# Optimization experiments

Measured on AMD Instinct MI355X. Metric: run time of the kernel, lower is better.

The kernel has to match this reference:

```python
import jax, jax.numpy as jnp
import numpy as np

B, VD, SD, CD, H, HEADS = 16384, 2048, 1024, 512, 256, 4
DH = H // HEADS
EPS = 1e-5


def layer_norm(x, g, b):
    m = jnp.mean(x, axis=-1, keepdims=True)
    v = jnp.var(x, axis=-1, keepdims=True)
    return (x - m) * jax.lax.rsqrt(v + EPS) * g + b


def setup_inputs() -> dict:
    key = jax.random.key(0)
    ks = jax.random.split(key, 16)
    sc = 0.02
    inp = {
        'fv': jax.random.normal(ks[0], (B, VD), jnp.float32),
        'fs': jax.random.normal(ks[1], (B, SD), jnp.float32),
        'fc': jax.random.normal(ks[2], (B, CD), jnp.float32),
        # projection linears + layernorms
        'Wv': jax.random.normal(ks[3], (H, VD), jnp.float32) * sc,
        'bv': jnp.zeros((H,), jnp.float32),
        'gv': jnp.ones((H,), jnp.float32), 'bev': jnp.zeros((H,), jnp.float32),
        'Ws': jax.random.normal(ks[4], (H, SD), jnp.float32) * sc,
        'bs': jnp.zeros((H,), jnp.float32),
        'gs': jnp.ones((H,), jnp.float32), 'bes': jnp.zeros((H,), jnp.float32),
        'Wc': jax.random.normal(ks[5], (H, CD), jnp.float32) * sc,
        'bc': jnp.zeros((H,), jnp.float32),
        'gc_': jnp.ones((H,), jnp.float32), 'bec': jnp.zeros((H,), jnp.float32),
        # MultiheadAttention packed in-proj and out-proj
        'in_w': jax.random.normal(ks[6], (3 * H, H), jnp.float32) * sc,
        'in_b': jnp.zeros((3 * H,), jnp.float32),
        'out_w': jax.random.normal(ks[7], (H, H), jnp.float32) * sc,
        'out_b': jnp.zeros((H,), jnp.float32),
        # post-attention layernorm
        'gn': jnp.ones((H,), jnp.float32), 'gb': jnp.zeros((H,), jnp.float32),
        # gating MLP: Linear(3H,64) -> GELU -> Linear(64,3) -> softmax
        'g1w': jax.random.normal(ks[8], (64, 3 * H), jnp.float32) * sc,
        'g1b': jnp.zeros((64,), jnp.float32),
        'g2w': jax.random.normal(ks[9], (3, 64), jnp.float32) * sc,
        'g2b': jnp.zeros((3,), jnp.float32),
    }
    return inp


def reference(fv, fs, fc, Wv, bv, gv, bev, Ws, bs, gs, bes, Wc, bc, gc_, bec,
              in_w, in_b, out_w, out_b, gn, gb, g1w, g1b, g2w, g2b):
    v = layer_norm(fv @ Wv.T + bv, gv, bev)   # [B,H]
    s = layer_norm(fs @ Ws.T + bs, gs, bes)
    c = layer_norm(fc @ Wc.T + bc, gc_, bec)
    stack = jnp.stack([v, s, c], axis=1)      # [B,3,H]

    # self-attention over seq=3 (eval mode: dropout off)
    qkv = stack @ in_w.T + in_b               # [B,3,3H]
    q, k, vv = jnp.split(qkv, 3, axis=-1)
    def heads(x):  # [B,3,H] -> [B,HEADS,3,DH]
        return x.reshape(B, 3, HEADS, DH).transpose(0, 2, 1, 3)
    q, k, vv = heads(q), heads(k), heads(vv)
    scores = jnp.einsum('bhqd,bhkd->bhqk', q, k) / jnp.sqrt(jnp.float32(DH))
    attn = jax.nn.softmax(scores, axis=-1)
    ctx = jnp.einsum('bhqk,bhkd->bhqd', attn, vv)
    ctx = ctx.transpose(0, 2, 1, 3).reshape(B, 3, H)
    attended = ctx @ out_w.T + out_b          # [B,3,H]

    attended = layer_norm(attended + stack, gn, gb)
    av, as_, ac = attended[:, 0], attended[:, 1], attended[:, 2]

    h1 = jax.nn.gelu(jnp.concatenate([av, as_, ac], axis=-1) @ g1w.T + g1b, approximate=False)
    gates = jax.nn.softmax(h1 @ g2w.T + g2b, axis=-1)  # [B,3]

    fused = gates[:, 0:1] * av + gates[:, 1:2] * as_ + gates[:, 2:3] * ac
    return (fused, gates)
```

## Files before the change

### kernel.cpp

```cpp
#include <hip/hip_runtime.h>
#include <math.h>


typedef unsigned short u16;
typedef __bf16 bf16x8 __attribute__((ext_vector_type(8)));
typedef float fx4 __attribute__((ext_vector_type(4)));

#define MFMA_BF16(A_, B_, C_) __builtin_amdgcn_mfma_f32_16x16x32_bf16((A_), (B_), (C_), 0, 0, 0)
#define WAIT_VM(N) asm volatile("s_waitcnt vmcnt(" #N ")" ::: "memory")

__device__ __forceinline__ float bf2f(u16 s) {
    union { float f; unsigned u; } c; c.u = ((unsigned)s) << 16; return c.f;
}
__device__ __forceinline__ u16 f2bf(float f) {
    union { float f; unsigned u; } c; c.f = f;
    return (u16)((c.u + 0x7fffu + ((c.u >> 16) & 1u)) >> 16);
}
__device__ __forceinline__ float bfpair_dot(unsigned a, unsigned b) {
    union { unsigned u; float f; } al, ah, bl, bh;
    al.u = a << 16; ah.u = a & 0xffff0000u;
    bl.u = b << 16; bh.u = b & 0xffff0000u;
    return al.f * bl.f + ah.f * bh.f;
}
__device__ __forceinline__ void gld16(void* l, const void* g) {
    __builtin_amdgcn_global_load_lds((const __attribute__((address_space(1))) void*)g,
                                     (__attribute__((address_space(3))) void*)l, 16, 0, 0);
}

__global__ __launch_bounds__(256) void cvt_w(const float* Wv, const float* Ws, const float* Wc,
                                             const float* inw, const float* outw, const float* g1w,
                                             u16* dst) {
    int idx = blockIdx.x * 256 + threadIdx.x;
    const float* src; int rel;
    if      (idx <  524288) { src = Wv;   rel = idx; }
    else if (idx <  786432) { src = Ws;   rel = idx -  524288; }
    else if (idx <  917504) { src = Wc;   rel = idx -  786432; }
    else if (idx < 1114112) { src = inw;  rel = idx -  917504; }
    else if (idx < 1179648) { src = outw; rel = idx - 1114112; }
    else                    { src = g1w;  rel = idx - 1179648; }
    dst[idx] = f2bf(src[rel]);
}

__global__ __launch_bounds__(256, 3) void gemm_ln(
    const float* fv, const float* fs, const float* fc,
    const u16* wWv, const u16* wWs, const u16* wWc,
    const float* bv, const float* gv, const float* bev,
    const float* bs, const float* gs, const float* bes,
    const float* bc, const float* gc_, const float* bec,
    u16* stack) {
    __shared__ alignas(16) char smem[45568];
    u16* sC = (u16*)smem;
    float* redS = (float*)(smem + 43008);
    float* redQ = (float*)(smem + 44032);
    float* mvS  = (float*)(smem + 45056);

    int bid = blockIdx.x;
    int slot, mblk;
    if (bid < 256)      { slot = 0; mblk = bid; }
    else if (bid < 512) { slot = 1; mblk = bid - 256; }
    else                { slot = 2; mblk = bid - 512; }

    const float* A; const u16* W; const float* bias; const float* gg; const float* be; int K;
    if (slot == 0)      { A = fv; W = wWv; bias = bv; gg = gv;  be = bev; K = 2048; }
    else if (slot == 1) { A = fs; W = wWs; bias = bs; gg = gs;  be = bes; K = 1024; }
    else                { A = fc; W = wWc; bias = bc; gg = gc_; be = bec; K = 512;  }

    int t = threadIdx.x, wv = t >> 6, ln = t & 63, q = ln >> 4, l15 = ln & 15;
    int m0 = mblk * 64;

    fx4 zero = {0.f, 0.f, 0.f, 0.f};
    fx4 acc[4][4];
    #pragma unroll
    for (int mi = 0; mi < 4; ++mi)
        #pragma unroll
        for (int ni = 0; ni < 4; ++ni) acc[mi][ni] = zero;

    int rowA = t >> 2, ca = t & 3;
    const float* aBase = A + (size_t)(m0 + rowA) * K + ca * 8;
    int sAwOff = rowA * 40 + ca * 8;

    int bN[4], bKc[4], bDst[4];
    #pragma unroll
    for (int i = 0; i < 4; ++i) {
        int d = wv * 256 + i * 64 + ln;
        bN[i] = d >> 2;
        bKc[i] = (d & 3) ^ ((bN[i] >> 1) & 3);
        bDst[i] = (wv * 256 + i * 64) * 16;
    }

    int niter = K >> 5;

    {
        float4 f0 = *(const float4*)(aBase);
        float4 f1 = *(const float4*)(aBase + 4);
        #pragma unroll
        for (int i = 0; i < 4; ++i)
            gld16(smem + 10240 + bDst[i], W + (size_t)bN[i] * K + bKc[i] * 8);
        union { u16 us[8]; uint4 v; } pk;
        pk.us[0] = f2bf(f0.x); pk.us[1] = f2bf(f0.y); pk.us[2] = f2bf(f0.z); pk.us[3] = f2bf(f0.w);
        pk.us[4] = f2bf(f1.x); pk.us[5] = f2bf(f1.y); pk.us[6] = f2bf(f1.z); pk.us[7] = f2bf(f1.w);
        *(uint4*)((u16*)smem + sAwOff) = pk.v;
    }
    __syncthreads();

    for (int kt = 0; kt < niter; ++kt) {
        int cur = kt & 1, nxt_b = (kt + 1) & 1;
        u16* sAc = (u16*)(smem + cur * 5120);
        u16* sBc = (u16*)(smem + 10240 + cur * 16384);
        int has_next = (kt + 1) < niter;

        float4 nf0, nf1;
        if (has_next) {
            nf0 = *(const float4*)(aBase + (kt + 1) * 32);
            nf1 = *(const float4*)(aBase + (kt + 1) * 32 + 4);
            char* sBn = smem + 10240 + nxt_b * 16384;
            #pragma unroll
            for (int i = 0; i < 4; ++i)
                gld16(sBn + bDst[i], W + (size_t)bN[i] * K + (kt + 1) * 32 + bKc[i] * 8);
        }

        bf16x8 af[4], bfr[4];
        #pragma unroll
        for (int mi = 0; mi < 4; ++mi)
            af[mi] = *(const bf16x8*)(sAc + (mi * 16 + l15) * 40 + q * 8);
        #pragma unroll
        for (int ni = 0; ni < 4; ++ni) {
            int n = wv * 64 + ni * 16 + l15;
            int ch = n * 4 + (q ^ ((n >> 1) & 3));
            bfr[ni] = *(const bf16x8*)(sBc + ch * 8);
        }
        #pragma unroll
        for (int mi = 0; mi < 4; ++mi)
            #pragma unroll
            for (int ni = 0; ni < 4; ++ni)
                acc[mi][ni] = MFMA_BF16(af[mi], bfr[ni], acc[mi][ni]);

        if (has_next) {
            union { u16 us[8]; uint4 v; } pk;
            pk.us[0] = f2bf(nf0.x); pk.us[1] = f2bf(nf0.y); pk.us[2] = f2bf(nf0.z); pk.us[3] = f2bf(nf0.w);
            pk.us[4] = f2bf(nf1.x); pk.us[5] = f2bf(nf1.y); pk.us[6] = f2bf(nf1.z); pk.us[7] = f2bf(nf1.w);
            *(uint4*)((u16*)(smem + nxt_b * 5120) + sAwOff) = pk.v;
        }
        __syncthreads();
    }

    float biasv[4], gvv[4], bevv[4];
    #pragma unroll
    for (int ni = 0; ni < 4; ++ni) {
        int col = wv * 64 + ni * 16 + l15;
        biasv[ni] = bias[col]; gvv[ni] = gg[col]; bevv[ni] = be[col];
    }
    #pragma unroll
    for (int mi = 0; mi < 4; ++mi)
        #pragma unroll
        for (int ni = 0; ni < 4; ++ni)
            #pragma unroll
            for (int r = 0; r < 4; ++r) acc[mi][ni][r] += biasv[ni];
    #pragma unroll
    for (int mi = 0; mi < 4; ++mi) {
        #pragma unroll
        for (int r = 0; r < 4; ++r) {
            float s = 0.f, qq = 0.f;
            #pragma unroll
            for (int ni = 0; ni < 4; ++ni) { float x = acc[mi][ni][r]; s += x; qq += x * x; }
            #pragma unroll
            for (int m = 1; m < 16; m <<= 1) { s += __shfl_xor(s, m, 64); qq += __shfl_xor(qq, m, 64); }
            if (l15 == 0) { int rho = mi * 16 + q * 4 + r; redS[rho * 4 + wv] = s; redQ[rho * 4 + wv] = qq; }
        }
    }
    __syncthreads();
    if (t < 64) {
        float s = redS[t * 4] + redS[t * 4 + 1] + redS[t * 4 + 2] + redS[t * 4 + 3];
        float qq = redQ[t * 4] + redQ[t * 4 + 1] + redQ[t * 4 + 2] + redQ[t * 4 + 3];
        float mean = s * (1.f / 256.f);
        float var = qq * (1.f / 256.f) - mean * mean;
        mvS[t * 2] = mean; mvS[t * 2 + 1] = rsqrtf(var + 1e-5f);
    }
    __syncthreads();
    #pragma unroll
    for (int mi = 0; mi < 4; ++mi) {
        #pragma unroll
        for (int r = 0; r < 4; ++r) {
            int rho = mi * 16 + q * 4 + r;
            float mean = mvS[rho * 2], rstd = mvS[rho * 2 + 1];
            #pragma unroll
            for (int ni = 0; ni < 4; ++ni) {
                int col = wv * 64 + ni * 16 + l15;
                float x = (acc[mi][ni][r] - mean) * rstd * gvv[ni] + bevv[ni];
                sC[rho * 256 + col] = f2bf(x);
            }
        }
    }
    __syncthreads();
    u16* outp = stack + (size_t)m0 * 768 + slot * 256;
    #pragma unroll
    for (int it = 0; it < 8; ++it) {
        int idx = t + it * 256;
        int row = idx >> 5, c = idx & 31;
        uint4 v = *(const uint4*)(sC + row * 256 + c * 8);
        *(uint4*)(outp + (size_t)row * 768 + c * 8) = v;
    }
}

__global__ __launch_bounds__(256, 3) void gemm_qkv(const u16* stack, const u16* W, const float* in_b,
                                                   u16* qkv) {
    __shared__ alignas(16) char smem[49152];
    u16* sC = (u16*)smem;

    int t = threadIdx.x, wv = t >> 6, ln = t & 63, q = ln >> 4, l15 = ln & 15;
    int n0 = blockIdx.x * 128, m0 = blockIdx.y * 128;
    int wr = wv >> 1, wc = wv & 1;

    fx4 zero = {0.f, 0.f, 0.f, 0.f};
    fx4 acc[4][4];
    #pragma unroll
    for (int mi = 0; mi < 4; ++mi)
        #pragma unroll
        for (int ni = 0; ni < 4; ++ni) acc[mi][ni] = zero;

    int sR[2], sKc[2];
    #pragma unroll
    for (int i = 0; i < 2; ++i) {
        int d = wv * 128 + i * 64 + ln;
        sR[i] = d >> 2;
        sKc[i] = (d & 3) ^ ((sR[i] >> 1) & 3);
    }

#define QK_ISSUE(ktile, bufoff)                                                         \
    {                                                                                   \
        char* bA_ = smem + (bufoff);                                                    \
        char* bB_ = bA_ + 8192;                                                         \
        _Pragma("unroll")                                                               \
        for (int i_ = 0; i_ < 2; ++i_) {                                                \
            gld16(bA_ + (wv * 128 + i_ * 64) * 16,                                      \
                  stack + (size_t)(m0 + sR[i_]) * 256 + (ktile) * 32 + sKc[i_] * 8);    \
            gld16(bB_ + (wv * 128 + i_ * 64) * 16,                                      \
                  W + (size_t)(n0 + sR[i_]) * 256 + (ktile) * 32 + sKc[i_] * 8);        \
        }                                                                               \
    }

    QK_ISSUE(0, 0);
    QK_ISSUE(1, 16384);
    int cb = 0;
    for (int kt = 0; kt < 8; ++kt) {
        if (kt < 7) { WAIT_VM(4); } else { WAIT_VM(0); }
        __builtin_amdgcn_sched_barrier(0);
        __builtin_amdgcn_s_barrier();
        __builtin_amdgcn_sched_barrier(0);
        int nb = cb + 2; if (nb >= 3) nb -= 3;
        if (kt + 2 < 8) QK_ISSUE(kt + 2, nb * 16384);

        const u16* sAc = (const u16*)(smem + cb * 16384);
        const u16* sBc = (const u16*)(smem + cb * 16384 + 8192);
        bf16x8 af[4], bfr[4];
        #pragma unroll
        for (int mi = 0; mi < 4; ++mi) {
            int r = wr * 64 + mi * 16 + l15;
            int ch = r * 4 + (q ^ ((r >> 1) & 3));
            af[mi] = *(const bf16x8*)(sAc + ch * 8);
        }
        #pragma unroll
        for (int ni = 0; ni < 4; ++ni) {
            int n = wc * 64 + ni * 16 + l15;
            int ch = n * 4 + (q ^ ((n >> 1) & 3));
            bfr[ni] = *(const bf16x8*)(sBc + ch * 8);
        }
        __builtin_amdgcn_s_setprio(1);
        #pragma unroll
        for (int mi = 0; mi < 4; ++mi)
            #pragma unroll
            for (int ni = 0; ni < 4; ++ni)
                acc[mi][ni] = MFMA_BF16(af[mi], bfr[ni], acc[mi][ni]);
        __builtin_amdgcn_s_setprio(0);
        cb += 1; if (cb >= 3) cb -= 3;
    }
#undef QK_ISSUE
    __syncthreads();

    float biasv[4];
    #pragma unroll
    for (int ni = 0; ni < 4; ++ni) biasv[ni] = in_b[n0 + wc * 64 + ni * 16 + l15];
    #pragma unroll
    for (int mi = 0; mi < 4; ++mi)
        #pragma unroll
        for (int ni = 0; ni < 4; ++ni)
            #pragma unroll
            for (int r = 0; r < 4; ++r) {
                int rl = wr * 64 + mi * 16 + q * 4 + r;
                int cl = wc * 64 + ni * 16 + l15;
                sC[rl * 128 + cl] = f2bf(acc[mi][ni][r] + biasv[ni]);
            }
    __syncthreads();
    #pragma unroll
    for (int it = 0; it < 8; ++it) {
        int idx = t + it * 256;
        int row = idx >> 4, c = idx & 15;
        uint4 v = *(const uint4*)(sC + row * 128 + c * 8);
        *(uint4*)(qkv + (size_t)(m0 + row) * 768 + n0 + c * 8) = v;
    }
}

__global__ __launch_bounds__(256) void outproj_k(
    const u16* qkv, const u16* W, const float* out_b, const u16* stack,
    const float* gn, const float* gb, const u16* g1w, const float* g1b,
    const float* g2w, const float* g2b, float* outF, float* outG) {
    __shared__ alignas(16) char smem[65536];
    u16* qk  = (u16*)smem;
    u16* vb  = (u16*)smem;
    u16* r1  = (u16*)(smem + 24576);
    u16* sB  = (u16*)(smem + 49152);
    float* sS   = (float*)(smem + 49152);
    float* redS = (float*)(smem + 49152);
    float* redQ = (float*)(smem + 49920);
    float* mvS  = (float*)(smem + 50688);
    float* h1S  = (float*)(smem + 51072);
    float* lgS  = (float*)(smem + 55168);
    float* gateS= (float*)(smem + 55360);

    int t = threadIdx.x, wv = t >> 6, ln = t & 63, q = ln >> 4, l15 = ln & 15;
    int gr0 = blockIdx.x * 48, b0 = blockIdx.x * 16;

    #pragma unroll
    for (int i = 0; i < 12; ++i) {
        int d = i * 256 + t;
        int row = d >> 6, cc = d & 63;
        gld16((char*)smem + d * 16, qkv + (size_t)(gr0 + row) * 768 + cc * 8);
    }
    __syncthreads();
    #pragma unroll
    for (int it = 0; it < 3; ++it) {
        int idx = t + it * 256;
        if (idx < 576) {
            int b = idx / 36, rem = idx % 36, h = rem / 9, pp = rem % 9, i = pp / 3, j = pp % 3;
            const u16* qp = qk + (b * 3 + i) * 512 + h * 64;
            const u16* kp = qk + (b * 3 + j) * 512 + 256 + h * 64;
            float acc = 0.f;
            #pragma unroll
            for (int c = 0; c < 8; ++c) {
                uint4 qa = *(const uint4*)(qp + c * 8);
                uint4 ka = *(const uint4*)(kp + c * 8);
                acc += bfpair_dot(qa.x, ka.x) + bfpair_dot(qa.y, ka.y) +
                       bfpair_dot(qa.z, ka.z) + bfpair_dot(qa.w, ka.w);
            }
            sS[idx] = acc * 0.125f;
        }
    }
    __syncthreads();
    #pragma unroll
    for (int i = 0; i < 6; ++i) {
        int d = i * 256 + t;
        int row = d >> 5, cc = d & 31;
        gld16((char*)smem + d * 16, qkv + (size_t)(gr0 + row) * 768 + 512 + cc * 8);
    }
    if (t < 192) {
        int b3 = t * 3;
        float s0 = sS[b3], s1 = sS[b3 + 1], s2 = sS[b3 + 2];
        float m = fmaxf(s0, fmaxf(s1, s2));
        float e0 = __expf(s0 - m), e1 = __expf(s1 - m), e2 = __expf(s2 - m);
        float inv = 1.f / (e0 + e1 + e2);
        sS[b3] = e0 * inv; sS[b3 + 1] = e1 * inv; sS[b3 + 2] = e2 * inv;
    }
    __syncthreads();
    #pragma unroll
    for (int it = 0; it < 6; ++it) {
        int idx = t + it * 256;
        int b = idx / 96, rem = idx % 96, i = rem / 32, c = rem & 31, h = c >> 3;
        int pbase = b * 36 + h * 9 + i * 3;
        float o[8];
        #pragma unroll
        for (int e = 0; e < 8; ++e) o[e] = 0.f;
        #pragma unroll
        for (int j = 0; j < 3; ++j) {
            float p = sS[pbase + j];
            uint4 va = *(const uint4*)(vb + (b * 3 + j) * 256 + c * 8);
            unsigned uu[4] = {va.x, va.y, va.z, va.w};
            #pragma unroll
            for (int pr = 0; pr < 4; ++pr) {
                union { unsigned u; float f; } lo, hi;
                lo.u = uu[pr] << 16; hi.u = uu[pr] & 0xffff0000u;
                o[2 * pr]     += p * lo.f;
                o[2 * pr + 1] += p * hi.f;
            }
        }
        union { u16 us[8]; uint4 v; } pk;
        #pragma unroll
        for (int e = 0; e < 8; ++e) pk.us[e] = f2bf(o[e]);
        int row = b * 3 + i;
        *(uint4*)(r1 + (row * 32 + (c ^ (row & 7))) * 8) = pk.v;
    }
    __syncthreads();

    fx4 zero = {0.f, 0.f, 0.f, 0.f};
    fx4 acc[3][4];
    #pragma unroll
    for (int mi = 0; mi < 3; ++mi)
        #pragma unroll
        for (int ni = 0; ni < 4; ++ni) acc[mi][ni] = zero;

    for (int kt = 0; kt < 8; ++kt) {
        #pragma unroll
        for (int i = 0; i < 4; ++i) {
            int d = wv * 256 + i * 64 + ln;
            int n = d >> 2, p = d & 3;
            int kc = p ^ ((n >> 1) & 3);
            gld16((char*)sB + (wv * 256 + i * 64) * 16, W + (size_t)n * 256 + kt * 32 + kc * 8);
        }
        __syncthreads();
        bf16x8 af[3], bfr[4];
        #pragma unroll
        for (int mi = 0; mi < 3; ++mi) {
            int row = mi * 16 + l15;
            int ch = row * 32 + ((kt * 4 + q) ^ (row & 7));
            af[mi] = *(const bf16x8*)(r1 + ch * 8);
        }
        #pragma unroll
        for (int ni = 0; ni < 4; ++ni) {
            int n = wv * 64 + ni * 16 + l15;
            int ch = n * 4 + (q ^ ((n >> 1) & 3));
            bfr[ni] = *(const bf16x8*)(sB + ch * 8);
        }
        #pragma unroll
        for (int mi = 0; mi < 3; ++mi)
            #pragma unroll
            for (int ni = 0; ni < 4; ++ni)
                acc[mi][ni] = MFMA_BF16(af[mi], bfr[ni], acc[mi][ni]);
        __syncthreads();
    }

    #pragma unroll
    for (int i = 0; i < 6; ++i) {
        int d = wv * 384 + i * 64 + ln;
        gld16((char*)r1 + (wv * 384 + i * 64) * 16, stack + (size_t)gr0 * 256 + (size_t)d * 8);
    }
    __syncthreads();

    float obv[4], gnv[4], gbv[4];
    #pragma unroll
    for (int ni = 0; ni < 4; ++ni) {
        int col = wv * 64 + ni * 16 + l15;
        obv[ni] = out_b[col]; gnv[ni] = gn[col]; gbv[ni] = gb[col];
    }
    #pragma unroll
    for (int mi = 0; mi < 3; ++mi)
        #pragma unroll
        for (int ni = 0; ni < 4; ++ni)
            #pragma unroll
            for (int r = 0; r < 4; ++r) {
                int rho = mi * 16 + q * 4 + r;
                int col = wv * 64 + ni * 16 + l15;
                acc[mi][ni][r] += obv[ni] + bf2f(r1[rho * 256 + col]);
            }
    #pragma unroll
    for (int mi = 0; mi < 3; ++mi) {
        #pragma unroll
        for (int r = 0; r < 4; ++r) {
            float s = 0.f, qq = 0.f;
            #pragma unroll
            for (int ni = 0; ni < 4; ++ni) { float x = acc[mi][ni][r]; s += x; qq += x * x; }
            #pragma unroll
            for (int m = 1; m < 16; m <<= 1) { s += __shfl_xor(s, m, 64); qq += __shfl_xor(qq, m, 64); }
            if (l15 == 0) { int rho = mi * 16 + q * 4 + r; redS[rho * 4 + wv] = s; redQ[rho * 4 + wv] = qq; }
        }
    }
    __syncthreads();
    if (t < 48) {
        float s = redS[t * 4] + redS[t * 4 + 1] + redS[t * 4 + 2] + redS[t * 4 + 3];
        float qq = redQ[t * 4] + redQ[t * 4 + 1] + redQ[t * 4 + 2] + redQ[t * 4 + 3];
        float mean = s * (1.f / 256.f);
        float var = qq * (1.f / 256.f) - mean * mean;
        mvS[t * 2] = mean; mvS[t * 2 + 1] = rsqrtf(var + 1e-5f);
    }
    __syncthreads();
    #pragma unroll
    for (int mi = 0; mi < 3; ++mi) {
        #pragma unroll
        for (int r = 0; r < 4; ++r) {
            int rho = mi * 16 + q * 4 + r;
            float mean = mvS[rho * 2], rstd = mvS[rho * 2 + 1];
            int bl = rho / 3, sl = rho - bl * 3;
            #pragma unroll
            for (int ni = 0; ni < 4; ++ni) {
                int col = wv * 64 + ni * 16 + l15;
                float x = (acc[mi][ni][r] - mean) * rstd * gnv[ni] + gbv[ni];
                int k = sl * 256 + col;
                int kidx = k >> 3, wn = k & 7;
                r1[(bl * 96 + (kidx ^ (bl & 7))) * 8 + wn] = f2bf(x);
            }
        }
    }
    __syncthreads();
    fx4 ag = zero;
    for (int kt = 0; kt < 24; ++kt) {
        int bl = l15;
        int kidx = kt * 4 + q;
        bf16x8 afr = *(const bf16x8*)(r1 + (bl * 96 + (kidx ^ (bl & 7))) * 8);
        int n = wv * 16 + l15;
        bf16x8 bfr2 = *(const bf16x8*)(g1w + (size_t)n * 768 + kt * 32 + q * 8);
        ag = MFMA_BF16(afr, bfr2, ag);
    }
    #pragma unroll
    for (int r = 0; r < 4; ++r) {
        int bl = q * 4 + r, n = wv * 16 + l15;
        float x = ag[r] + g1b[n];
        h1S[bl * 64 + n] = 0.5f * x * (1.f + erff(x * 0.70710678118f));
    }
    __syncthreads();
    if (t < 48) {
        int bl = t / 3, s = t - bl * 3;
        float a = g2b[s];
        #pragma unroll
        for (int k = 0; k < 64; ++k) a += h1S[bl * 64 + k] * g2w[s * 64 + k];
        lgS[t] = a;
    }
    __syncthreads();
    if (t < 48) {
        int bl = t / 3, s = t - bl * 3;
        float l0 = lgS[bl * 3], l1 = lgS[bl * 3 + 1], l2 = lgS[bl * 3 + 2];
        float m = fmaxf(l0, fmaxf(l1, l2));
        float e0 = __expf(l0 - m), e1 = __expf(l1 - m), e2 = __expf(l2 - m);
        float inv = 1.f / (e0 + e1 + e2);
        float gsel = ((s == 0) ? e0 : (s == 1) ? e1 : e2) * inv;
        gateS[t] = gsel;
        outG[(size_t)(b0 + bl) * 3 + s] = gsel;
    }
    __syncthreads();
    #pragma unroll
    for (int it = 0; it < 2; ++it) {
        int idx = t + it * 256;
        int b = idx >> 5, c = idx & 31;
        float g0 = gateS[b * 3], g1 = gateS[b * 3 + 1], g2 = gateS[b * 3 + 2];
        float o[8];
        #pragma unroll
        for (int e = 0; e < 8; ++e) o[e] = 0.f;
        #pragma unroll
        for (int s = 0; s < 3; ++s) {
            float gw = (s == 0) ? g0 : (s == 1) ? g1 : g2;
            int kidx = s * 32 + c;
            uint4 raw = *(const uint4*)(r1 + (b * 96 + (kidx ^ (b & 7))) * 8);
            unsigned uu[4] = {raw.x, raw.y, raw.z, raw.w};
            #pragma unroll
            for (int pr = 0; pr < 4; ++pr) {
                union { unsigned u; float f; } lo, hi;
                lo.u = uu[pr] << 16; hi.u = uu[pr] & 0xffff0000u;
                o[2 * pr]     += gw * lo.f;
                o[2 * pr + 1] += gw * hi.f;
            }
        }
        float* op = outF + (size_t)(b0 + b) * 256 + c * 8;
        float4 v0; v0.x = o[0]; v0.y = o[1]; v0.z = o[2]; v0.w = o[3];
        float4 v1; v1.x = o[4]; v1.y = o[5]; v1.z = o[6]; v1.w = o[7];
        *(float4*)op = v0;
        *(float4*)(op + 4) = v1;
    }
}

extern "C" void kernel_launch(void* const* d_in, const int* in_sizes, int n_in,
                              void* d_out, int out_size, void* d_ws, size_t ws_size,
                              hipStream_t stream) {
    (void)in_sizes; (void)n_in; (void)out_size; (void)ws_size;
    const float* fv   = (const float*)d_in[0];
    const float* fs   = (const float*)d_in[1];
    const float* fc   = (const float*)d_in[2];
    const float* Wv   = (const float*)d_in[3];
    const float* bv   = (const float*)d_in[4];
    const float* gv   = (const float*)d_in[5];
    const float* bev  = (const float*)d_in[6];
    const float* Ws   = (const float*)d_in[7];
    const float* bs   = (const float*)d_in[8];
    const float* gs   = (const float*)d_in[9];
    const float* bes  = (const float*)d_in[10];
    const float* Wc   = (const float*)d_in[11];
    const float* bc   = (const float*)d_in[12];
    const float* gc_  = (const float*)d_in[13];
    const float* bec  = (const float*)d_in[14];
    const float* in_w = (const float*)d_in[15];
    const float* in_b = (const float*)d_in[16];
    const float* out_w= (const float*)d_in[17];
    const float* out_b= (const float*)d_in[18];
    const float* gn   = (const float*)d_in[19];
    const float* gb   = (const float*)d_in[20];
    const float* g1w  = (const float*)d_in[21];
    const float* g1b  = (const float*)d_in[22];
    const float* g2w  = (const float*)d_in[23];
    const float* g2b  = (const float*)d_in[24];

    u16* w0    = (u16*)d_ws;
    u16* wWv   = w0;
    u16* wWs   = w0 + 524288;
    u16* wWc   = w0 + 786432;
    u16* wIn   = w0 + 917504;
    u16* wOut  = w0 + 1114112;
    u16* wG1   = w0 + 1179648;
    u16* stack = w0 + 1228800;
    u16* qkv   = w0 + 13811712;
    float* outF = (float*)d_out;
    float* outG = outF + (size_t)16384 * 256;

    cvt_w<<<4800, 256, 0, stream>>>(Wv, Ws, Wc, in_w, out_w, g1w, w0);
    gemm_ln<<<768, 256, 0, stream>>>(fv, fs, fc, wWv, wWs, wWc,
                                     bv, gv, bev, bs, gs, bes, bc, gc_, bec, stack);
    gemm_qkv<<<dim3(6, 384), 256, 0, stream>>>(stack, wIn, in_b, qkv);
    outproj_k<<<1024, 256, 0, stream>>>(qkv, wOut, out_b, stack, gn, gb,
                                        wG1, g1b, g2w, g2b, outF, outG);
}
```

Before: 421.2 us.

## Fuse QKV projection GEMM into attention/out-proj kernel, removing qkv round-trip

Removes the separate gemm_qkv kernel and computes the QKV projection for each 48-row tile inside outproj_k, keeping q/k/v in LDS instead of writing and re-reading a bf16 qkv buffer in global memory. The block grows to 512 threads with ~146KB LDS, and the in-proj and out-proj weight slices are streamed through a triple-buffered async pipeline. The stack tile is loaded once and reused for the residual. The trade-off is that every block re-reads the full in_w matrix (from L2) and occupancy drops to one block per CU because of the large LDS footprint.

```diff
diff --git a/kernel.cpp b/kernel.cpp
--- a/kernel.cpp
+++ b/kernel.cpp
@@ -202,134 +202,136 @@
     }
 }
 
-__global__ __launch_bounds__(256, 3) void gemm_qkv(const u16* stack, const u16* W, const float* in_b,
-                                                   u16* qkv) {
-    __shared__ alignas(16) char smem[49152];
-    u16* sC = (u16*)smem;
-
-    int t = threadIdx.x, wv = t >> 6, ln = t & 63, q = ln >> 4, l15 = ln & 15;
-    int n0 = blockIdx.x * 128, m0 = blockIdx.y * 128;
-    int wr = wv >> 1, wc = wv & 1;
-
-    fx4 zero = {0.f, 0.f, 0.f, 0.f};
-    fx4 acc[4][4];
-    #pragma unroll
-    for (int mi = 0; mi < 4; ++mi)
-        #pragma unroll
-        for (int ni = 0; ni < 4; ++ni) acc[mi][ni] = zero;
-
-    int sR[2], sKc[2];
-    #pragma unroll
-    for (int i = 0; i < 2; ++i) {
-        int d = wv * 128 + i * 64 + ln;
-        sR[i] = d >> 2;
-        sKc[i] = (d & 3) ^ ((sR[i] >> 1) & 3);
-    }
-
-#define QK_ISSUE(ktile, bufoff)                                                         \
-    {                                                                                   \
-        char* bA_ = smem + (bufoff);                                                    \
-        char* bB_ = bA_ + 8192;                                                         \
-        _Pragma("unroll")                                                               \
-        for (int i_ = 0; i_ < 2; ++i_) {                                                \
-            gld16(bA_ + (wv * 128 + i_ * 64) * 16,                                      \
-                  stack + (size_t)(m0 + sR[i_]) * 256 + (ktile) * 32 + sKc[i_] * 8);    \
-            gld16(bB_ + (wv * 128 + i_ * 64) * 16,                                      \
-                  W + (size_t)(n0 + sR[i_]) * 256 + (ktile) * 32 + sKc[i_] * 8);        \
-        }                                                                               \
-    }
-
-    QK_ISSUE(0, 0);
-    QK_ISSUE(1, 16384);
-    int cb = 0;
-    for (int kt = 0; kt < 8; ++kt) {
-        if (kt < 7) { WAIT_VM(4); } else { WAIT_VM(0); }
-        __builtin_amdgcn_sched_barrier(0);
-        __builtin_amdgcn_s_barrier();
-        __builtin_amdgcn_sched_barrier(0);
-        int nb = cb + 2; if (nb >= 3) nb -= 3;
-        if (kt + 2 < 8) QK_ISSUE(kt + 2, nb * 16384);
-
-        const u16* sAc = (const u16*)(smem + cb * 16384);
-        const u16* sBc = (const u16*)(smem + cb * 16384 + 8192);
-        bf16x8 af[4], bfr[4];
-        #pragma unroll
-        for (int mi = 0; mi < 4; ++mi) {
-            int r = wr * 64 + mi * 16 + l15;
-            int ch = r * 4 + (q ^ ((r >> 1) & 3));
-            af[mi] = *(const bf16x8*)(sAc + ch * 8);
-        }
-        #pragma unroll
-        for (int ni = 0; ni < 4; ++ni) {
-            int n = wc * 64 + ni * 16 + l15;
-            int ch = n * 4 + (q ^ ((n >> 1) & 3));
-            bfr[ni] = *(const bf16x8*)(sBc + ch * 8);
-        }
-        __builtin_amdgcn_s_setprio(1);
-        #pragma unroll
-        for (int mi = 0; mi < 4; ++mi)
-            #pragma unroll
-            for (int ni = 0; ni < 4; ++ni)
-                acc[mi][ni] = MFMA_BF16(af[mi], bfr[ni], acc[mi][ni]);
-        __builtin_amdgcn_s_setprio(0);
-        cb += 1; if (cb >= 3) cb -= 3;
-    }
-#undef QK_ISSUE
-    __syncthreads();
-
-    float biasv[4];
-    #pragma unroll
-    for (int ni = 0; ni < 4; ++ni) biasv[ni] = in_b[n0 + wc * 64 + ni * 16 + l15];
-    #pragma unroll
-    for (int mi = 0; mi < 4; ++mi)
-        #pragma unroll
-        for (int ni = 0; ni < 4; ++ni)
-            #pragma unroll
-            for (int r = 0; r < 4; ++r) {
-                int rl = wr * 64 + mi * 16 + q * 4 + r;
-                int cl = wc * 64 + ni * 16 + l15;
-                sC[rl * 128 + cl] = f2bf(acc[mi][ni][r] + biasv[ni]);
-            }
-    __syncthreads();
-    #pragma unroll
-    for (int it = 0; it < 8; ++it) {
-        int idx = t + it * 256;
-        int row = idx >> 4, c = idx & 15;
-        uint4 v = *(const uint4*)(sC + row * 128 + c * 8);
-        *(uint4*)(qkv + (size_t)(m0 + row) * 768 + n0 + c * 8) = v;
-    }
-}
-
-__global__ __launch_bounds__(256) void outproj_k(
-    const u16* qkv, const u16* W, const float* out_b, const u16* stack,
+__global__ __launch_bounds__(512) void outproj_k(
+    const u16* stack, const u16* Win, const float* in_b,
+    const u16* W, const float* out_b,
     const float* gn, const float* gb, const u16* g1w, const float* g1b,
     const float* g2w, const float* g2b, float* outF, float* outG) {
-    __shared__ alignas(16) char smem[65536];
-    u16* qk  = (u16*)smem;
-    u16* vb  = (u16*)smem;
+    __shared__ alignas(16) char smem[149760];
+    u16* stackS = (u16*)smem;
+    u16* qk  = (u16*)(smem + 24576);
     u16* r1  = (u16*)(smem + 24576);
-    u16* sB  = (u16*)(smem + 49152);
-    float* sS   = (float*)(smem + 49152);
-    float* redS = (float*)(smem + 49152);
-    float* redQ = (float*)(smem + 49920);
-    float* mvS  = (float*)(smem + 50688);
-    float* h1S  = (float*)(smem + 51072);
-    float* lgS  = (float*)(smem + 55168);
-    float* gateS= (float*)(smem + 55360);
+    u16* vb  = (u16*)(smem + 73728);
+    float* sS   = (float*)(smem + 147456);
+    float* redS = (float*)(smem + 73728);
+    float* redQ = (float*)(smem + 75264);
+    float* mvS  = (float*)(smem + 76800);
+    float* h1S  = (float*)(smem + 77184);
+    float* lgS  = (float*)(smem + 81280);
+    float* gateS= (float*)(smem + 81472);
 
     int t = threadIdx.x, wv = t >> 6, ln = t & 63, q = ln >> 4, l15 = ln & 15;
     int gr0 = blockIdx.x * 48, b0 = blockIdx.x * 16;
 
-    #pragma unroll
-    for (int i = 0; i < 12; ++i) {
-        int d = i * 256 + t;
-        int row = d >> 6, cc = d & 63;
-        gld16((char*)smem + d * 16, qkv + (size_t)(gr0 + row) * 768 + cc * 8);
-    }
-    __syncthreads();
-    #pragma unroll
-    for (int it = 0; it < 3; ++it) {
-        int idx = t + it * 256;
+    int stR[3], stKc[3];
+    #pragma unroll
+    for (int i = 0; i < 3; ++i) {
+        int d = i * 512 + t;
+        stR[i] = d >> 5;
+        stKc[i] = (d & 31) ^ (stR[i] & 7);
+    }
+    int bN[2], bKc[2];
+    #pragma unroll
+    for (int i = 0; i < 2; ++i) {
+        int d = i * 512 + t;
+        bN[i] = d >> 2;
+        bKc[i] = (d & 3) ^ ((bN[i] >> 1) & 3);
+    }
+
+#define SLICE_IN(s_, buf_)                                                            \
+    {                                                                                 \
+        int np_ = (s_) >> 3, kt_ = (s_) & 7;                                          \
+        char* dst_ = smem + 98304 + (buf_) * 16384;                                   \
+        _Pragma("unroll")                                                             \
+        for (int i_ = 0; i_ < 2; ++i_)                                                \
+            gld16(dst_ + (i_ * 512 + t) * 16,                                         \
+                  Win + (size_t)(np_ * 256 + bN[i_]) * 256 + kt_ * 32 + bKc[i_] * 8); \
+    }
+#define SLICE_OUT(kt_, buf_)                                                          \
+    {                                                                                 \
+        char* dst_ = smem + 98304 + (buf_) * 16384;                                   \
+        _Pragma("unroll")                                                             \
+        for (int i_ = 0; i_ < 2; ++i_)                                                \
+            gld16(dst_ + (i_ * 512 + t) * 16,                                         \
+                  W + (size_t)bN[i_] * 256 + (kt_) * 32 + bKc[i_] * 8);               \
+    }
+
+    fx4 zero = {0.f, 0.f, 0.f, 0.f};
+
+    #pragma unroll
+    for (int i = 0; i < 3; ++i)
+        gld16((char*)stackS + (i * 512 + t) * 16,
+              stack + (size_t)(gr0 + stR[i]) * 256 + stKc[i] * 8);
+    SLICE_IN(0, 0);
+    SLICE_IN(1, 1);
+
+    {
+        fx4 acc[3][2];
+        #pragma unroll
+        for (int mi = 0; mi < 3; ++mi)
+            #pragma unroll
+            for (int ni = 0; ni < 2; ++ni) acc[mi][ni] = zero;
+
+        int cb = 0;
+        for (int s = 0; s < 24; ++s) {
+            if (s < 23) { WAIT_VM(2); } else { WAIT_VM(0); }
+            __builtin_amdgcn_sched_barrier(0);
+            __builtin_amdgcn_s_barrier();
+            __builtin_amdgcn_sched_barrier(0);
+            int nb = cb + 2; if (nb >= 3) nb -= 3;
+            if (s + 2 < 24) SLICE_IN(s + 2, nb);
+
+            int kt = s & 7;
+            const u16* sBc = (const u16*)(smem + 98304 + cb * 16384);
+            bf16x8 af[3], bfr[2];
+            #pragma unroll
+            for (int mi = 0; mi < 3; ++mi) {
+                int row = mi * 16 + l15;
+                af[mi] = *(const bf16x8*)(stackS + (row * 32 + ((kt * 4 + q) ^ (row & 7))) * 8);
+            }
+            #pragma unroll
+            for (int ni = 0; ni < 2; ++ni) {
+                int n = wv * 32 + ni * 16 + l15;
+                int ch = n * 4 + (q ^ ((n >> 1) & 3));
+                bfr[ni] = *(const bf16x8*)(sBc + ch * 8);
+            }
+            __builtin_amdgcn_s_setprio(1);
+            #pragma unroll
+            for (int mi = 0; mi < 3; ++mi)
+                #pragma unroll
+                for (int ni = 0; ni < 2; ++ni)
+                    acc[mi][ni] = MFMA_BF16(af[mi], bfr[ni], acc[mi][ni]);
+            __builtin_amdgcn_s_setprio(0);
+
+            if (kt == 7) {
+                int np = s >> 3;
+                #pragma unroll
+                for (int ni = 0; ni < 2; ++ni) {
+                    int cl = wv * 32 + ni * 16 + l15;
+                    float bias = in_b[np * 256 + cl];
+                    #pragma unroll
+                    for (int mi = 0; mi < 3; ++mi)
+                        #pragma unroll
+                        for (int r = 0; r < 4; ++r) {
+                            int rl = mi * 16 + q * 4 + r;
+                            u16 val = f2bf(acc[mi][ni][r] + bias);
+                            if (np < 2) qk[rl * 512 + np * 256 + cl] = val;
+                            else        vb[rl * 256 + cl] = val;
+                        }
+                }
+                #pragma unroll
+                for (int mi = 0; mi < 3; ++mi)
+                    #pragma unroll
+                    for (int ni = 0; ni < 2; ++ni) acc[mi][ni] = zero;
+            }
+            cb += 1; if (cb >= 3) cb -= 3;
+        }
+    }
+    __syncthreads();
+
+    #pragma unroll
+    for (int it = 0; it < 2; ++it) {
+        int idx = t + it * 512;
         if (idx < 576) {
             int b = idx / 36, rem = idx % 36, h = rem / 9, pp = rem % 9, i = pp / 3, j = pp % 3;
             const u16* qp = qk + (b * 3 + i) * 512 + h * 64;
@@ -346,12 +348,6 @@
         }
     }
     __syncthreads();
-    #pragma unroll
-    for (int i = 0; i < 6; ++i) {
-        int d = i * 256 + t;
-        int row = d >> 5, cc = d & 31;
-        gld16((char*)smem + d * 16, qkv + (size_t)(gr0 + row) * 768 + 512 + cc * 8);
-    }
     if (t < 192) {
         int b3 = t * 3;
         float s0 = sS[b3], s1 = sS[b3 + 1], s2 = sS[b3 + 2];
@@ -362,8 +358,8 @@
     }
     __syncthreads();
     #pragma unroll
-    for (int it = 0; it < 6; ++it) {
-        int idx = t + it * 256;
+    for (int it = 0; it < 3; ++it) {
+        int idx = t + it * 512;
         int b = idx / 96, rem = idx % 96, i = rem / 32, c = rem & 31, h = c >> 3;
         int pbase = b * 36 + h * 9 + i * 3;
         float o[8];
@@ -390,65 +386,65 @@
     }
     __syncthreads();
 
-    fx4 zero = {0.f, 0.f, 0.f, 0.f};
-    fx4 acc[3][4];
+    fx4 acc2[3][2];
     #pragma unroll
     for (int mi = 0; mi < 3; ++mi)
         #pragma unroll
-        for (int ni = 0; ni < 4; ++ni) acc[mi][ni] = zero;
-
-    for (int kt = 0; kt < 8; ++kt) {
-        #pragma unroll
-        for (int i = 0; i < 4; ++i) {
-            int d = wv * 256 + i * 64 + ln;
-            int n = d >> 2, p = d & 3;
-            int kc = p ^ ((n >> 1) & 3);
-            gld16((char*)sB + (wv * 256 + i * 64) * 16, W + (size_t)n * 256 + kt * 32 + kc * 8);
-        }
-        __syncthreads();
-        bf16x8 af[3], bfr[4];
-        #pragma unroll
-        for (int mi = 0; mi < 3; ++mi) {
-            int row = mi * 16 + l15;
-            int ch = row * 32 + ((kt * 4 + q) ^ (row & 7));
-            af[mi] = *(const bf16x8*)(r1 + ch * 8);
-        }
-        #pragma unroll
-        for (int ni = 0; ni < 4; ++ni) {
-            int n = wv * 64 + ni * 16 + l15;
-            int ch = n * 4 + (q ^ ((n >> 1) & 3));
-            bfr[ni] = *(const bf16x8*)(sB + ch * 8);
-        }
-        #pragma unroll
-        for (int mi = 0; mi < 3; ++mi)
-            #pragma unroll
-            for (int ni = 0; ni < 4; ++ni)
-                acc[mi][ni] = MFMA_BF16(af[mi], bfr[ni], acc[mi][ni]);
-        __syncthreads();
-    }
-
-    #pragma unroll
-    for (int i = 0; i < 6; ++i) {
-        int d = wv * 384 + i * 64 + ln;
-        gld16((char*)r1 + (wv * 384 + i * 64) * 16, stack + (size_t)gr0 * 256 + (size_t)d * 8);
-    }
-    __syncthreads();
-
-    float obv[4], gnv[4], gbv[4];
-    #pragma unroll
-    for (int ni = 0; ni < 4; ++ni) {
-        int col = wv * 64 + ni * 16 + l15;
+        for (int ni = 0; ni < 2; ++ni) acc2[mi][ni] = zero;
+
+    SLICE_OUT(0, 0);
+    SLICE_OUT(1, 1);
+    {
+        int cb = 0;
+        for (int kt = 0; kt < 8; ++kt) {
+            if (kt < 7) { WAIT_VM(2); } else { WAIT_VM(0); }
+            __builtin_amdgcn_sched_barrier(0);
+            __builtin_amdgcn_s_barrier();
+            __builtin_amdgcn_sched_barrier(0);
+            int nb = cb + 2; if (nb >= 3) nb -= 3;
+            if (kt + 2 < 8) SLICE_OUT(kt + 2, nb);
+
+            const u16* sBc = (const u16*)(smem + 98304 + cb * 16384);
+            bf16x8 af[3], bfr[2];
+            #pragma unroll
+            for (int mi = 0; mi < 3; ++mi) {
+                int row = mi * 16 + l15;
+                af[mi] = *(const bf16x8*)(r1 + (row * 32 + ((kt * 4 + q) ^ (row & 7))) * 8);
+            }
+            #pragma unroll
+            for (int ni = 0; ni < 2; ++ni) {
+                int n = wv * 32 + ni * 16 + l15;
+                int ch = n * 4 + (q ^ ((n >> 1) & 3));
+                bfr[ni] = *(const bf16x8*)(sBc + ch * 8);
+            }
+            __builtin_amdgcn_s_setprio(1);
+            #pragma unroll
+            for (int mi = 0; mi < 3; ++mi)
+                #pragma unroll
+                for (int ni = 0; ni < 2; ++ni)
+                    acc2[mi][ni] = MFMA_BF16(af[mi], bfr[ni], acc2[mi][ni]);
+            __builtin_amdgcn_s_setprio(0);
+            cb += 1; if (cb >= 3) cb -= 3;
+        }
+    }
+    __syncthreads();
+
+    float obv[2], gnv[2], gbv[2];
+    #pragma unroll
+    for (int ni = 0; ni < 2; ++ni) {
+        int col = wv * 32 + ni * 16 + l15;
         obv[ni] = out_b[col]; gnv[ni] = gn[col]; gbv[ni] = gb[col];
     }
     #pragma unroll
     for (int mi = 0; mi < 3; ++mi)
         #pragma unroll
-        for (int ni = 0; ni < 4; ++ni)
+        for (int ni = 0; ni < 2; ++ni)
             #pragma unroll
             for (int r = 0; r < 4; ++r) {
                 int rho = mi * 16 + q * 4 + r;
-                int col = wv * 64 + ni * 16 + l15;
-                acc[mi][ni][r] += obv[ni] + bf2f(r1[rho * 256 + col]);
+                int col = wv * 32 + ni * 16 + l15;
+                u16 sv = stackS[(rho * 32 + ((col >> 3) ^ (rho & 7))) * 8 + (col & 7)];
+                acc2[mi][ni][r] += obv[ni] + bf2f(sv);
             }
     #pragma unroll
     for (int mi = 0; mi < 3; ++mi) {
@@ -456,16 +452,17 @@
         for (int r = 0; r < 4; ++r) {
             float s = 0.f, qq = 0.f;
             #pragma unroll
-            for (int ni = 0; ni < 4; ++ni) { float x = acc[mi][ni][r]; s += x; qq += x * x; }
+            for (int ni = 0; ni < 2; ++ni) { float x = acc2[mi][ni][r]; s += x; qq += x * x; }
             #pragma unroll
             for (int m = 1; m < 16; m <<= 1) { s += __shfl_xor(s, m, 64); qq += __shfl_xor(qq, m, 64); }
-            if (l15 == 0) { int rho = mi * 16 + q * 4 + r; redS[rho * 4 + wv] = s; redQ[rho * 4 + wv] = qq; }
+            if (l15 == 0) { int rho = mi * 16 + q * 4 + r; redS[rho * 8 + wv] = s; redQ[rho * 8 + wv] = qq; }
         }
     }
     __syncthreads();
     if (t < 48) {
-        float s = redS[t * 4] + redS[t * 4 + 1] + redS[t * 4 + 2] + redS[t * 4 + 3];
-        float qq = redQ[t * 4] + redQ[t * 4 + 1] + redQ[t * 4 + 2] + redQ[t * 4 + 3];
+        float s = 0.f, qq = 0.f;
+        #pragma unroll
+        for (int i = 0; i < 8; ++i) { s += redS[t * 8 + i]; qq += redQ[t * 8 + i]; }
         float mean = s * (1.f / 256.f);
         float var = qq * (1.f / 256.f) - mean * mean;
         mvS[t * 2] = mean; mvS[t * 2 + 1] = rsqrtf(var + 1e-5f);
@@ -479,9 +476,9 @@
             float mean = mvS[rho * 2], rstd = mvS[rho * 2 + 1];
             int bl = rho / 3, sl = rho - bl * 3;
             #pragma unroll
-            for (int ni = 0; ni < 4; ++ni) {
-                int col = wv * 64 + ni * 16 + l15;
-                float x = (acc[mi][ni][r] - mean) * rstd * gnv[ni] + gbv[ni];
+            for (int ni = 0; ni < 2; ++ni) {
+                int col = wv * 32 + ni * 16 + l15;
+                float x = (acc2[mi][ni][r] - mean) * rstd * gnv[ni] + gbv[ni];
                 int k = sl * 256 + col;
                 int kidx = k >> 3, wn = k & 7;
                 r1[(bl * 96 + (kidx ^ (bl & 7))) * 8 + wn] = f2bf(x);
@@ -489,20 +486,22 @@
         }
     }
     __syncthreads();
-    fx4 ag = zero;
-    for (int kt = 0; kt < 24; ++kt) {
-        int bl = l15;
-        int kidx = kt * 4 + q;
-        bf16x8 afr = *(const bf16x8*)(r1 + (bl * 96 + (kidx ^ (bl & 7))) * 8);
-        int n = wv * 16 + l15;
-        bf16x8 bfr2 = *(const bf16x8*)(g1w + (size_t)n * 768 + kt * 32 + q * 8);
-        ag = MFMA_BF16(afr, bfr2, ag);
-    }
-    #pragma unroll
-    for (int r = 0; r < 4; ++r) {
-        int bl = q * 4 + r, n = wv * 16 + l15;
-        float x = ag[r] + g1b[n];
-        h1S[bl * 64 + n] = 0.5f * x * (1.f + erff(x * 0.70710678118f));
+    if (wv < 4) {
+        fx4 ag = zero;
+        for (int kt = 0; kt < 24; ++kt) {
+            int bl = l15;
+            int kidx = kt * 4 + q;
+            bf16x8 afr = *(const bf16x8*)(r1 + (bl * 96 + (kidx ^ (bl & 7))) * 8);
+            int n = wv * 16 + l15;
+            bf16x8 bfr2 = *(const bf16x8*)(g1w + (size_t)n * 768 + kt * 32 + q * 8);
+            ag = MFMA_BF16(afr, bfr2, ag);
+        }
+        #pragma unroll
+        for (int r = 0; r < 4; ++r) {
+            int bl = q * 4 + r, n = wv * 16 + l15;
+            float x = ag[r] + g1b[n];
+            h1S[bl * 64 + n] = 0.5f * x * (1.f + erff(x * 0.70710678118f));
+        }
     }
     __syncthreads();
     if (t < 48) {
@@ -524,10 +523,8 @@
         outG[(size_t)(b0 + bl) * 3 + s] = gsel;
     }
     __syncthreads();
-    #pragma unroll
-    for (int it = 0; it < 2; ++it) {
-        int idx = t + it * 256;
-        int b = idx >> 5, c = idx & 31;
+    {
+        int b = t >> 5, c = t & 31;
         float g0 = gateS[b * 3], g1 = gateS[b * 3 + 1], g2 = gateS[b * 3 + 2];
         float o[8];
         #pragma unroll
@@ -552,6 +549,8 @@
         *(float4*)op = v0;
         *(float4*)(op + 4) = v1;
     }
+#undef SLICE_IN
+#undef SLICE_OUT
 }
 
 extern "C" void kernel_launch(void* const* d_in, const int* in_sizes, int n_in,
@@ -592,14 +591,12 @@
     u16* wOut  = w0 + 1114112;
     u16* wG1   = w0 + 1179648;
     u16* stack = w0 + 1228800;
-    u16* qkv   = w0 + 13811712;
     float* outF = (float*)d_out;
     float* outG = outF + (size_t)16384 * 256;
 
     cvt_w<<<4800, 256, 0, stream>>>(Wv, Ws, Wc, in_w, out_w, g1w, w0);
     gemm_ln<<<768, 256, 0, stream>>>(fv, fs, fc, wWv, wWs, wWc,
                                      bv, gv, bev, bs, gs, bes, bc, gc_, bec, stack);
-    gemm_qkv<<<dim3(6, 384), 256, 0, stream>>>(stack, wIn, in_b, qkv);
-    outproj_k<<<1024, 256, 0, stream>>>(qkv, wOut, out_b, stack, gn, gb,
+    outproj_k<<<1024, 512, 0, stream>>>(stack, wIn, in_b, wOut, out_b, gn, gb,
                                         wG1, g1b, g2w, g2b, outF, outG);
 }
```

Result: slower. 444.9 us (+5.6%).

## Load A fragments directly into registers, bypassing LDS staging in gemm_ln

Applied to the files above, without the earlier changes.

Each wave now loads the fp32 activation rows it needs for its MFMA A-fragments straight from global memory and converts them to bf16 in registers. This removes the A tile in shared memory along with its write and read round trip, and shrinks LDS use. The cost is that all four waves in a block load the same A data redundantly, giving four times the global/L2 A traffic, and more registers are needed to prefetch 8 float4 values per thread.

```diff
diff --git a/kernel.cpp b/kernel.cpp
--- a/kernel.cpp
+++ b/kernel.cpp
@@ -48,11 +48,11 @@
     const float* bs, const float* gs, const float* bes,
     const float* bc, const float* gc_, const float* bec,
     u16* stack) {
-    __shared__ alignas(16) char smem[45568];
+    __shared__ alignas(16) char smem[35328];
     u16* sC = (u16*)smem;
-    float* redS = (float*)(smem + 43008);
-    float* redQ = (float*)(smem + 44032);
-    float* mvS  = (float*)(smem + 45056);
+    float* redS = (float*)(smem + 32768);
+    float* redQ = (float*)(smem + 33792);
+    float* mvS  = (float*)(smem + 34816);
 
     int bid = blockIdx.x;
     int slot, mblk;
@@ -75,9 +75,10 @@
         #pragma unroll
         for (int ni = 0; ni < 4; ++ni) acc[mi][ni] = zero;
 
-    int rowA = t >> 2, ca = t & 3;
-    const float* aBase = A + (size_t)(m0 + rowA) * K + ca * 8;
-    int sAwOff = rowA * 40 + ca * 8;
+    const float* aRow[4];
+    #pragma unroll
+    for (int mi = 0; mi < 4; ++mi)
+        aRow[mi] = A + (size_t)(m0 + mi * 16 + l15) * K + q * 8;
 
     int bN[4], bKc[4], bDst[4];
     #pragma unroll
@@ -90,39 +91,44 @@
 
     int niter = K >> 5;
 
-    {
-        float4 f0 = *(const float4*)(aBase);
-        float4 f1 = *(const float4*)(aBase + 4);
-        #pragma unroll
-        for (int i = 0; i < 4; ++i)
-            gld16(smem + 10240 + bDst[i], W + (size_t)bN[i] * K + bKc[i] * 8);
-        union { u16 us[8]; uint4 v; } pk;
-        pk.us[0] = f2bf(f0.x); pk.us[1] = f2bf(f0.y); pk.us[2] = f2bf(f0.z); pk.us[3] = f2bf(f0.w);
-        pk.us[4] = f2bf(f1.x); pk.us[5] = f2bf(f1.y); pk.us[6] = f2bf(f1.z); pk.us[7] = f2bf(f1.w);
-        *(uint4*)((u16*)smem + sAwOff) = pk.v;
+    bf16x8 faf[4];
+    float4 pa0[4], pa1[4];
+
+    #pragma unroll
+    for (int mi = 0; mi < 4; ++mi) {
+        pa0[mi] = *(const float4*)(aRow[mi]);
+        pa1[mi] = *(const float4*)(aRow[mi] + 4);
+    }
+    #pragma unroll
+    for (int i = 0; i < 4; ++i)
+        gld16(smem + bDst[i], W + (size_t)bN[i] * K + bKc[i] * 8);
+    #pragma unroll
+    for (int mi = 0; mi < 4; ++mi) {
+        faf[mi][0] = (__bf16)pa0[mi].x; faf[mi][1] = (__bf16)pa0[mi].y;
+        faf[mi][2] = (__bf16)pa0[mi].z; faf[mi][3] = (__bf16)pa0[mi].w;
+        faf[mi][4] = (__bf16)pa1[mi].x; faf[mi][5] = (__bf16)pa1[mi].y;
+        faf[mi][6] = (__bf16)pa1[mi].z; faf[mi][7] = (__bf16)pa1[mi].w;
     }
     __syncthreads();
 
     for (int kt = 0; kt < niter; ++kt) {
         int cur = kt & 1, nxt_b = (kt + 1) & 1;
-        u16* sAc = (u16*)(smem + cur * 5120);
-        u16* sBc = (u16*)(smem + 10240 + cur * 16384);
+        const u16* sBc = (const u16*)(smem + cur * 16384);
         int has_next = (kt + 1) < niter;
 
-        float4 nf0, nf1;
         if (has_next) {
-            nf0 = *(const float4*)(aBase + (kt + 1) * 32);
-            nf1 = *(const float4*)(aBase + (kt + 1) * 32 + 4);
-            char* sBn = smem + 10240 + nxt_b * 16384;
+            #pragma unroll
+            for (int mi = 0; mi < 4; ++mi) {
+                pa0[mi] = *(const float4*)(aRow[mi] + (kt + 1) * 32);
+                pa1[mi] = *(const float4*)(aRow[mi] + (kt + 1) * 32 + 4);
+            }
+            char* sBn = smem + nxt_b * 16384;
             #pragma unroll
             for (int i = 0; i < 4; ++i)
                 gld16(sBn + bDst[i], W + (size_t)bN[i] * K + (kt + 1) * 32 + bKc[i] * 8);
         }
 
-        bf16x8 af[4], bfr[4];
-        #pragma unroll
-        for (int mi = 0; mi < 4; ++mi)
-            af[mi] = *(const bf16x8*)(sAc + (mi * 16 + l15) * 40 + q * 8);
+        bf16x8 bfr[4];
         #pragma unroll
         for (int ni = 0; ni < 4; ++ni) {
             int n = wv * 64 + ni * 16 + l15;
@@ -133,13 +139,16 @@
         for (int mi = 0; mi < 4; ++mi)
             #pragma unroll
             for (int ni = 0; ni < 4; ++ni)
-                acc[mi][ni] = MFMA_BF16(af[mi], bfr[ni], acc[mi][ni]);
+                acc[mi][ni] = MFMA_BF16(faf[mi], bfr[ni], acc[mi][ni]);
 
         if (has_next) {
-            union { u16 us[8]; uint4 v; } pk;
-            pk.us[0] = f2bf(nf0.x); pk.us[1] = f2bf(nf0.y); pk.us[2] = f2bf(nf0.z); pk.us[3] = f2bf(nf0.w);
-            pk.us[4] = f2bf(nf1.x); pk.us[5] = f2bf(nf1.y); pk.us[6] = f2bf(nf1.z); pk.us[7] = f2bf(nf1.w);
-            *(uint4*)((u16*)(smem + nxt_b * 5120) + sAwOff) = pk.v;
+            #pragma unroll
+            for (int mi = 0; mi < 4; ++mi) {
+                faf[mi][0] = (__bf16)pa0[mi].x; faf[mi][1] = (__bf16)pa0[mi].y;
+                faf[mi][2] = (__bf16)pa0[mi].z; faf[mi][3] = (__bf16)pa0[mi].w;
+                faf[mi][4] = (__bf16)pa1[mi].x; faf[mi][5] = (__bf16)pa1[mi].y;
+                faf[mi][6] = (__bf16)pa1[mi].z; faf[mi][7] = (__bf16)pa1[mi].w;
+            }
         }
         __syncthreads();
     }
```

Result: slower. 473.6 us (+12.4%).
